# Kernel tuning notes

Hardware: AMD Instinct MI355X
Metric: run time of the kernel (lower is better)

Reference implementation:

```python
import jax, jax.numpy as jnp
import numpy as np

B, N = 16384, 4096
NBLOCKS = 4
BLK = N // NBLOCKS  # 1024


def setup_inputs() -> dict:
    key = jax.random.key(0)
    kx, k1, k2, kb = jax.random.split(key, 4)
    # match torch kaiming-style uniform bounds approximately; exact init values
    # don't affect correctness testing, scale kept modest for stability
    bound_w = float(np.sqrt(3.0) * (np.sqrt(2.0 / (1 + 5)) / np.sqrt(BLK)))
    bound_b = 1.0 / float(np.sqrt(N))
    x = jax.random.normal(kx, (B, N), dtype=jnp.float32)
    w1 = jax.random.uniform(k1, (NBLOCKS, BLK, BLK), jnp.float32, -bound_w, bound_w)
    w2 = jax.random.uniform(k2, (NBLOCKS, BLK, BLK), jnp.float32, -bound_w, bound_w)
    bias = jax.random.uniform(kb, (N,), jnp.float32, -bound_b, bound_b)
    return {"x": x, "w1": w1, "w2": w2, "bias": bias}


def monarch_matmul(x, w1, w2):
    # x: (B, n); w1: (k, q, p) with k*p = n; w2: (l, s, r) with l*r = k*q
    Bd, n = x.shape
    k, q, p = w1.shape
    l, s, r = w2.shape
    # out1[b,k,q] = sum_p x[b,k,p] * w1[k,q,p]
    out1 = jnp.einsum('bkp,kqp->bkq', x.reshape(Bd, k, p), w1)
    # permute (k*q) flat -> (r, l), then transpose to (l, r)
    t = out1.reshape(Bd, r, l).transpose(0, 2, 1)  # (B, l, r)
    # out2[b,l,s] = sum_r t[b,l,r] * w2[l,s,r]
    out2 = jnp.einsum('blr,lsr->bls', t, w2)
    # permute to (B, s, l) then flatten -> (B, s*l)
    return out2.transpose(0, 2, 1).reshape(Bd, s * l)


def reference(x, w1, w2, bias):
    return monarch_matmul(x, w1, w2) + bias
```

## Files before the change

kernel.cpp:

```cpp
#include <hip/hip_runtime.h>
#include <hip/hip_bf16.h>
#include <stdint.h>

typedef __bf16 bf16_t;
typedef bf16_t bf16x8 __attribute__((ext_vector_type(8)));
typedef bf16_t bf16x4 __attribute__((ext_vector_type(4)));
typedef float  f32x4  __attribute__((ext_vector_type(4)));

#define B_DIM 16384

#define BAR()    __builtin_amdgcn_s_barrier()
#define SCHED0() __builtin_amdgcn_sched_barrier(0)
#define LGKM0()  asm volatile("s_waitcnt lgkmcnt(0)" ::: "memory")
#define VMCNT6() asm volatile("s_waitcnt vmcnt(6)" ::: "memory")
#define VMCNT0() asm volatile("s_waitcnt vmcnt(0)" ::: "memory")

__device__ __forceinline__ void async_copy16(void* lptr, const void* gptr) {
  __builtin_amdgcn_global_load_lds(
      (const __attribute__((address_space(1))) unsigned int*)gptr,
      (__attribute__((address_space(3))) unsigned int*)lptr, 16, 0, 0);
}

__global__ void cast_all_kernel(const float* __restrict__ x, const float* __restrict__ w1,
                                const float* __restrict__ w2, bf16_t* __restrict__ xb,
                                bf16_t* __restrict__ w1b, bf16_t* __restrict__ w2b) {
  size_t c = (size_t)blockIdx.x * 256 + threadIdx.x;
  const float* s; bf16_t* d; size_t off;
  if (c < 8388608)      { s = x;  d = xb;  off = c; }
  else if (c < 8912896) { s = w1; d = w1b; off = c - 8388608; }
  else                  { s = w2; d = w2b; off = c - 8912896; }
  size_t i = off * 8;
  f32x4 a = *(const f32x4*)(s + i);
  f32x4 b = *(const f32x4*)(s + i + 4);
  bf16x8 o;
  o[0]=(bf16_t)a[0]; o[1]=(bf16_t)a[1]; o[2]=(bf16_t)a[2]; o[3]=(bf16_t)a[3];
  o[4]=(bf16_t)b[0]; o[5]=(bf16_t)b[1]; o[6]=(bf16_t)b[2]; o[7]=(bf16_t)b[3];
  *(bf16x8*)(d + i) = o;
}

template<int EPI>
__global__ __launch_bounds__(512, 2)
void monarch_gemm8(const bf16_t* __restrict__ Ab, const bf16_t* __restrict__ Wb,
                   bf16_t* __restrict__ Outb)
{
  __shared__ __align__(16) char smem[131072];
  const int tid  = threadIdx.x;
  const int lane = tid & 63;
  const int wid  = tid >> 6;
  const int wm   = wid >> 2;
  const int wn   = wid & 3;

  const int pb = blockIdx.x;
  const int lb = (pb & 7) * 128 + (pb >> 3);
  const int zi = lb >> 8;
  const int mt = (lb & 255) >> 2;
  const int nt = lb & 3;

  const size_t brow0 = (size_t)mt * 256;
  const int    ncol0 = nt * 256;

  const bf16_t* Asrc = Ab + brow0 * 4096 + (size_t)zi * 1024;
  const bf16_t* Bsrc = Wb + ((size_t)zi << 20) + (size_t)ncol0 * 1024;

  const int sRow = lane >> 3;
  const int sC   = (lane & 7) ^ sRow;

  auto stage = [&](int t, int h) {
    const int ldsBase = (t & 1) * 65536 + (h >> 1) * 32768 + (h & 1) * 16384;
    const bf16_t* src = (h < 2) ? (Asrc + (size_t)(h * 128) * 4096 + t * 64)
                                : (Bsrc + (size_t)((h - 2) * 128) * 1024 + t * 64);
    const size_t strideE = (h < 2) ? 4096 : 1024;
    #pragma unroll
    for (int j = 0; j < 2; ++j) {
      const int row = j * 64 + wid * 8 + sRow;
      async_copy16(smem + ldsBase + j * 8192 + wid * 1024,
                   src + (size_t)row * strideE + sC * 8);
    }
  };

  const int cs0 = ((0 + (lane >> 4)) ^ (lane & 7)) * 16;
  const int cs1 = ((4 + (lane >> 4)) ^ (lane & 7)) * 16;
  const int aBase = (wm * 128 + (lane & 15)) * 128;
  const int bBase = 32768 + (wn * 64 + (lane & 15)) * 128;

#define RDA(buf, m, kk) (*(const bf16x8*)(smem + (buf)*65536 + aBase + (m)*2048 + ((kk)?cs1:cs0)))
#define RDB(buf, n, kk) (*(const bf16x8*)(smem + (buf)*65536 + bBase + (n)*2048 + ((kk)?cs1:cs0)))

  f32x4 acc[8][4] = {};
  bf16x8 aM0[4][2], aM1[4][2], bN0[2][2], bN1[2][2];

#define MFMA_QUAD(AR, Aarr, NB, Barr)                                              \
  __builtin_amdgcn_s_setprio(1);                                                   \
  _Pragma("unroll") for (int m = 0; m < 4; ++m)                                    \
  _Pragma("unroll") for (int n = 0; n < 2; ++n)                                    \
  _Pragma("unroll") for (int kk = 0; kk < 2; ++kk)                                 \
    acc[(AR)+m][(NB)+n] = __builtin_amdgcn_mfma_f32_16x16x32_bf16(                 \
        Aarr[m][kk], Barr[n][kk], acc[(AR)+m][(NB)+n], 0, 0, 0);                   \
  __builtin_amdgcn_s_setprio(0);

  stage(0,0); stage(0,1); stage(0,2); stage(0,3);
  stage(1,0); stage(1,1); stage(1,2);
  VMCNT6(); SCHED0(); BAR();

  for (int it2 = 0; it2 < 8; ++it2) {
    const int t0 = it2 * 2;
    const bool notlast = (it2 < 7);
    #pragma unroll
    for (int m = 0; m < 4; ++m) { aM0[m][0] = RDA(0,m,0); aM0[m][1] = RDA(0,m,1); }
    #pragma unroll
    for (int n = 0; n < 2; ++n) { bN0[n][0] = RDB(0,n,0); bN0[n][1] = RDB(0,n,1); }
    stage(t0+1, 3);
    SCHED0(); BAR(); LGKM0(); SCHED0();
    MFMA_QUAD(0, aM0, 0, bN0);
    SCHED0(); BAR();
    #pragma unroll
    for (int m = 0; m < 4; ++m) { aM1[m][0] = RDA(0,m+4,0); aM1[m][1] = RDA(0,m+4,1); }
    #pragma unroll
    for (int n = 0; n < 2; ++n) { bN1[n][0] = RDB(0,n+2,0); bN1[n][1] = RDB(0,n+2,1); }
    SCHED0(); BAR(); LGKM0(); SCHED0();
    MFMA_QUAD(0, aM0, 2, bN1);
    SCHED0(); BAR();
    if (notlast) stage(t0+2, 0);
    SCHED0(); BAR();
    MFMA_QUAD(4, aM1, 2, bN1);
    SCHED0(); BAR();
    if (notlast) { stage(t0+2, 1); stage(t0+2, 2); VMCNT6(); }
    else         { VMCNT0(); }
    SCHED0(); BAR();
    MFMA_QUAD(4, aM1, 0, bN0);
    SCHED0(); BAR();
    #pragma unroll
    for (int m = 0; m < 4; ++m) { aM0[m][0] = RDA(1,m,0); aM0[m][1] = RDA(1,m,1); }
    #pragma unroll
    for (int n = 0; n < 2; ++n) { bN0[n][0] = RDB(1,n,0); bN0[n][1] = RDB(1,n,1); }
    if (notlast) stage(t0+2, 3);
    SCHED0(); BAR(); LGKM0(); SCHED0();
    MFMA_QUAD(0, aM0, 0, bN0);
    SCHED0(); BAR();
    #pragma unroll
    for (int m = 0; m < 4; ++m) { aM1[m][0] = RDA(1,m+4,0); aM1[m][1] = RDA(1,m+4,1); }
    #pragma unroll
    for (int n = 0; n < 2; ++n) { bN1[n][0] = RDB(1,n+2,0); bN1[n][1] = RDB(1,n+2,1); }
    SCHED0(); BAR(); LGKM0(); SCHED0();
    MFMA_QUAD(0, aM0, 2, bN1);
    SCHED0(); BAR();
    if (notlast) stage(t0+3, 0);
    SCHED0(); BAR();
    MFMA_QUAD(4, aM1, 2, bN1);
    SCHED0(); BAR();
    if (notlast) { stage(t0+3, 1); stage(t0+3, 2); VMCNT6(); }
    SCHED0(); BAR();
    MFMA_QUAD(4, aM1, 0, bN0);
    SCHED0(); BAR();
  }

  bf16_t* C = (bf16_t*)smem;
  #pragma unroll
  for (int half = 0; half < 2; ++half) {
    BAR();
    if (wm == half) {
      const int rg = lane >> 4, cl = lane & 15;
      #pragma unroll
      for (int m = 0; m < 8; ++m)
        #pragma unroll
        for (int n = 0; n < 4; ++n) {
          const int rl = m * 16 + rg * 4;
          const int col = wn * 64 + n * 16 + cl;
          #pragma unroll
          for (int j = 0; j < 4; ++j)
            C[(rl + j) * 264 + col] = (bf16_t)acc[m][n][j];
        }
    }
    BAR();
    if (EPI == 0) {
      #pragma unroll
      for (int i = 0; i < 8; ++i) {
        const int s = i * 512 + tid;
        const int row = s >> 5, l = (s >> 3) & 3, part = s & 7;
        bf16x8 v;
        #pragma unroll
        for (int u = 0; u < 8; ++u) v[u] = C[row * 264 + l + 4 * (part * 8 + u)];
        *(bf16x8*)&Outb[(brow0 + half * 128 + row) * 4096 +
                        l * 1024 + zi * 256 + nt * 64 + part * 8] = v;
      }
    } else {
      #pragma unroll
      for (int i = 0; i < 8; ++i) {
        const int s = i * 512 + tid;
        const int row = s >> 5, ch = s & 31;
        bf16x8 v = *(const bf16x8*)&C[row * 264 + ch * 8];
        *(bf16x8*)&Outb[(brow0 + half * 128 + row) * 4096 +
                        (size_t)zi * 1024 + ncol0 + ch * 8] = v;
      }
    }
  }
#undef RDA
#undef RDB
#undef MFMA_QUAD
}

__global__ void permute_bias_kernel(const bf16_t* __restrict__ o2,
                                    const float* __restrict__ bias,
                                    float* __restrict__ out) {
  const int t = blockIdx.x * 256 + threadIdx.x;
  const int b = t >> 8;
  const int s0 = (t & 255) * 4;
  const size_t rowb = (size_t)b * 4096;
  bf16x4 vl[4];
  #pragma unroll
  for (int l = 0; l < 4; ++l) vl[l] = *(const bf16x4*)(o2 + rowb + l * 1024 + s0);
  #pragma unroll
  for (int si = 0; si < 4; ++si) {
    f32x4 bb = *(const f32x4*)(bias + (size_t)(s0 + si) * 4);
    f32x4 o;
    o[0] = (float)vl[0][si] + bb[0];
    o[1] = (float)vl[1][si] + bb[1];
    o[2] = (float)vl[2][si] + bb[2];
    o[3] = (float)vl[3][si] + bb[3];
    *(f32x4*)(out + rowb + (size_t)(s0 + si) * 4) = o;
  }
}

extern "C" void kernel_launch(void* const* d_in, const int* in_sizes, int n_in,
                              void* d_out, int out_size, void* d_ws, size_t ws_size,
                              hipStream_t stream) {
  const float* x    = (const float*)d_in[0];
  const float* w1   = (const float*)d_in[1];
  const float* w2   = (const float*)d_in[2];
  const float* bias = (const float*)d_in[3];
  float* out = (float*)d_out;

  char* ws = (char*)d_ws;
  const size_t xbBytes    = (size_t)B_DIM * 4096 * 2;
  const size_t wBytes     = (size_t)8 << 20;
  bf16_t* xb    = (bf16_t*)(ws);
  bf16_t* w1b   = (bf16_t*)(ws + xbBytes);
  bf16_t* w2b   = (bf16_t*)(ws + xbBytes + wBytes);
  bf16_t* inter = (bf16_t*)(ws + xbBytes + 2 * wBytes);
  bf16_t* o2    = xb;

  cast_all_kernel<<<36864, 256, 0, stream>>>(x, w1, w2, xb, w1b, w2b);
  monarch_gemm8<0><<<1024, 512, 0, stream>>>(xb, w1b, inter);
  monarch_gemm8<1><<<1024, 512, 0, stream>>>(inter, w2b, o2);
  permute_bias_kernel<<<16384, 256, 0, stream>>>(o2, bias, out);
}
```

Before: 516.3 us.

## Reorder MFMA quadrants and prefetch B fragments across iterations in GEMM loop

Changes the order of MFMA quadrants within each k-step to A0B0, A1B0, A0B1, A1B1. B-fragment LDS reads are hoisted so they overlap the preceding MFMA block, and the next buffer's B0 fragments are loaded during the last quadrant of the previous step. It also replaces the builtin barrier plus sched_barrier pairs with an inline-asm s_barrier carrying a memory clobber. The goal is to hide LDS read latency behind MFMA work and cut scheduling fences. The cost is tighter register lifetimes and a risk of reading LDS data that is still being overwritten, if the new barrier placement does not cover every hazard.

```diff
diff --git a/kernel.cpp b/kernel.cpp
--- a/kernel.cpp
+++ b/kernel.cpp
@@ -9,7 +9,7 @@
 
 #define B_DIM 16384
 
-#define BAR()    __builtin_amdgcn_s_barrier()
+#define BARM()   asm volatile("s_barrier" ::: "memory")
 #define SCHED0() __builtin_amdgcn_sched_barrier(0)
 #define LGKM0()  asm volatile("s_waitcnt lgkmcnt(0)" ::: "memory")
 #define VMCNT6() asm volatile("s_waitcnt vmcnt(6)" ::: "memory")
@@ -98,66 +98,68 @@
         Aarr[m][kk], Barr[n][kk], acc[(AR)+m][(NB)+n], 0, 0, 0);                   \
   __builtin_amdgcn_s_setprio(0);
 
+#define LD_A0(buf) _Pragma("unroll") for (int m = 0; m < 4; ++m) { \
+    aM0[m][0] = RDA(buf,m,0); aM0[m][1] = RDA(buf,m,1); }
+#define LD_A1(buf) _Pragma("unroll") for (int m = 0; m < 4; ++m) { \
+    aM1[m][0] = RDA(buf,m+4,0); aM1[m][1] = RDA(buf,m+4,1); }
+#define LD_B0(buf) _Pragma("unroll") for (int n = 0; n < 2; ++n) { \
+    bN0[n][0] = RDB(buf,n,0); bN0[n][1] = RDB(buf,n,1); }
+#define LD_B1(buf) _Pragma("unroll") for (int n = 0; n < 2; ++n) { \
+    bN1[n][0] = RDB(buf,n+2,0); bN1[n][1] = RDB(buf,n+2,1); }
+
   stage(0,0); stage(0,1); stage(0,2); stage(0,3);
   stage(1,0); stage(1,1); stage(1,2);
-  VMCNT6(); SCHED0(); BAR();
+  VMCNT6(); BARM();
+  LD_B0(0);
 
   for (int it2 = 0; it2 < 8; ++it2) {
     const int t0 = it2 * 2;
     const bool notlast = (it2 < 7);
-    #pragma unroll
-    for (int m = 0; m < 4; ++m) { aM0[m][0] = RDA(0,m,0); aM0[m][1] = RDA(0,m,1); }
-    #pragma unroll
-    for (int n = 0; n < 2; ++n) { bN0[n][0] = RDB(0,n,0); bN0[n][1] = RDB(0,n,1); }
+    LD_A0(0);
     stage(t0+1, 3);
-    SCHED0(); BAR(); LGKM0(); SCHED0();
+    BARM(); LGKM0(); SCHED0();
     MFMA_QUAD(0, aM0, 0, bN0);
-    SCHED0(); BAR();
-    #pragma unroll
-    for (int m = 0; m < 4; ++m) { aM1[m][0] = RDA(0,m+4,0); aM1[m][1] = RDA(0,m+4,1); }
-    #pragma unroll
-    for (int n = 0; n < 2; ++n) { bN1[n][0] = RDB(0,n+2,0); bN1[n][1] = RDB(0,n+2,1); }
-    SCHED0(); BAR(); LGKM0(); SCHED0();
+    BARM();
+    LD_A1(0);
+    BARM(); LGKM0(); SCHED0();
+    MFMA_QUAD(4, aM1, 0, bN0);
+    BARM();
+    LD_B1(0);
+    if (notlast) stage(t0+2, 0);
+    BARM(); LGKM0(); SCHED0();
     MFMA_QUAD(0, aM0, 2, bN1);
-    SCHED0(); BAR();
-    if (notlast) stage(t0+2, 0);
-    SCHED0(); BAR();
-    MFMA_QUAD(4, aM1, 2, bN1);
-    SCHED0(); BAR();
+    BARM();
     if (notlast) { stage(t0+2, 1); stage(t0+2, 2); VMCNT6(); }
     else         { VMCNT0(); }
-    SCHED0(); BAR();
+    BARM();
+    LD_B0(1);
+    MFMA_QUAD(4, aM1, 2, bN1);
+    BARM();
+    LD_A0(1);
+    if (notlast) stage(t0+2, 3);
+    BARM(); LGKM0(); SCHED0();
+    MFMA_QUAD(0, aM0, 0, bN0);
+    BARM();
+    LD_A1(1);
+    BARM(); LGKM0(); SCHED0();
     MFMA_QUAD(4, aM1, 0, bN0);
-    SCHED0(); BAR();
-    #pragma unroll
-    for (int m = 0; m < 4; ++m) { aM0[m][0] = RDA(1,m,0); aM0[m][1] = RDA(1,m,1); }
-    #pragma unroll
-    for (int n = 0; n < 2; ++n) { bN0[n][0] = RDB(1,n,0); bN0[n][1] = RDB(1,n,1); }
-    if (notlast) stage(t0+2, 3);
-    SCHED0(); BAR(); LGKM0(); SCHED0();
-    MFMA_QUAD(0, aM0, 0, bN0);
-    SCHED0(); BAR();
-    #pragma unroll
-    for (int m = 0; m < 4; ++m) { aM1[m][0] = RDA(1,m+4,0); aM1[m][1] = RDA(1,m+4,1); }
-    #pragma unroll
-    for (int n = 0; n < 2; ++n) { bN1[n][0] = RDB(1,n+2,0); bN1[n][1] = RDB(1,n+2,1); }
-    SCHED0(); BAR(); LGKM0(); SCHED0();
+    BARM();
+    LD_B1(1);
+    if (notlast) stage(t0+3, 0);
+    BARM(); LGKM0(); SCHED0();
     MFMA_QUAD(0, aM0, 2, bN1);
-    SCHED0(); BAR();
-    if (notlast) stage(t0+3, 0);
-    SCHED0(); BAR();
+    BARM();
+    if (notlast) { stage(t0+3, 1); stage(t0+3, 2); VMCNT6(); }
+    BARM();
+    if (notlast) { LD_B0(0); }
     MFMA_QUAD(4, aM1, 2, bN1);
-    SCHED0(); BAR();
-    if (notlast) { stage(t0+3, 1); stage(t0+3, 2); VMCNT6(); }
-    SCHED0(); BAR();
-    MFMA_QUAD(4, aM1, 0, bN0);
-    SCHED0(); BAR();
+    BARM();
   }
 
   bf16_t* C = (bf16_t*)smem;
   #pragma unroll
   for (int half = 0; half < 2; ++half) {
-    BAR();
+    BARM();
     if (wm == half) {
       const int rg = lane >> 4, cl = lane & 15;
       #pragma unroll
@@ -171,7 +173,7 @@
             C[(rl + j) * 264 + col] = (bf16_t)acc[m][n][j];
         }
     }
-    BAR();
+    BARM();
     if (EPI == 0) {
       #pragma unroll
       for (int i = 0; i < 8; ++i) {
@@ -197,6 +199,10 @@
 #undef RDA
 #undef RDB
 #undef MFMA_QUAD
+#undef LD_A0
+#undef LD_A1
+#undef LD_B0
+#undef LD_B1
 }
 
 __global__ void permute_bias_kernel(const bf16_t* __restrict__ o2,
```

Result: faster. 491.6 us (-4.8%).
